# Optimization experiments

Hardware: AMD Instinct MI355X
Metric: run time of the kernel (lower is better)

The kernel has to match this reference:

```python
import jax, jax.numpy as jnp
import numpy as np

B, NPG, D = 512, 200, 256  # graphs, nodes-per-graph, d_model
N = B * NPG
STEP = 4


def setup_inputs() -> dict:
    key = jax.random.key(0)
    ks = jax.random.split(key, 7)
    def xav(k, shape):
        fan_in, fan_out = shape[1], shape[0]
        std = float(np.sqrt(2.0 / (fan_in + fan_out)))
        return jax.random.normal(k, shape, jnp.float32) * std
    return {
        "node": jax.random.normal(ks[0], (N, D), jnp.float32),
        "node_num": jnp.full((B,), NPG, dtype=jnp.int32),
        "W_ih": xav(ks[1], (4 * D, 2 * D)),  # lstm weight_ih_l0
        "W_hh": xav(ks[2], (4 * D, D)),      # lstm weight_hh_l0
        "b_ih": jnp.zeros((4 * D,), jnp.float32),
        "b_hh": jnp.zeros((4 * D,), jnp.float32),
        "Wo": xav(ks[3], (D, 2 * D)),        # W_o.weight
        "bo": jnp.zeros((D,), jnp.float32),  # W_o.bias
    }


def reference(node, node_num, W_ih, W_hh, b_ih, b_hh, Wo, bo):
    n_total, d = node.shape
    bsz = node_num.shape[0]
    batch_idx = jnp.repeat(jnp.arange(bsz), node_num, total_repeat_length=n_total)
    h = jnp.zeros((bsz, d), node.dtype)
    c = jnp.zeros((bsz, d), node.dtype)
    q_star = jnp.zeros((bsz, 2 * d), node.dtype)
    for _ in range(STEP):
        # single-step LSTM (torch gate order: i, f, g, o)
        gates = q_star @ W_ih.T + h @ W_hh.T + b_ih + b_hh
        i, f, g, o = jnp.split(gates, 4, axis=-1)
        c = jax.nn.sigmoid(f) * c + jax.nn.sigmoid(i) * jnp.tanh(g)
        h = jax.nn.sigmoid(o) * jnp.tanh(c)
        q = h  # [B, d]
        # segmented softmax attention over nodes
        e = jnp.sum(node * q[batch_idx], axis=-1)  # [N]
        emax = jax.ops.segment_max(e, batch_idx, num_segments=bsz)
        e = jnp.exp(e - emax[batch_idx])
        denom = jax.ops.segment_sum(e, batch_idx, num_segments=bsz)
        a = e / (denom[batch_idx] + 1e-6)
        r = jax.ops.segment_sum(a[:, None] * node, batch_idx, num_segments=bsz)
        q_star = jnp.concatenate([q, r], axis=-1)
    return q_star @ Wo.T + bo
```

## Files before the change

kernel.cpp:

```cpp
#include <hip/hip_runtime.h>
#include <math.h>

#define DCH 256
#define BSZ 512
#define NPG 200
#define G4  1024
#define K2  512
#define KSD 4

typedef __attribute__((ext_vector_type(8))) short short8v;
typedef __attribute__((ext_vector_type(4))) float f32x4;

__device__ __forceinline__ float sigf(float x) { return 1.0f / (1.0f + __expf(-x)); }

__device__ __forceinline__ unsigned pack2bf(float a, float b) {
    unsigned ua = __float_as_uint(a), ub = __float_as_uint(b);
    ua = (ua + 0x7FFFu + ((ua >> 16) & 1u)) >> 16;
    ub = (ub + 0x7FFFu + ((ub >> 16) & 1u)) & 0xFFFF0000u;
    return ua | ub;
}
__device__ __forceinline__ float lo_bf(unsigned u) { return __uint_as_float(u << 16); }
__device__ __forceinline__ float hi_bf(unsigned u) { return __uint_as_float(u & 0xFFFF0000u); }

__global__ __launch_bounds__(256) void gemm_gates_mfma(
    const unsigned short* __restrict__ hrbf,
    const unsigned short* __restrict__ wcat,
    float* __restrict__ gpart, int Kper)
{
    const int wid  = threadIdx.x >> 6;
    const int lane = threadIdx.x & 63;
    const int gx = blockIdx.x * 128 + wid * 32;
    const int gm = blockIdx.y * 64;
    const int kbase = blockIdx.z * Kper;
    const int rsel = lane & 15, kgrp = lane >> 4;

    f32x4 a0m0 = {}, a0m1 = {}, a0m2 = {}, a0m3 = {},
          a1m0 = {}, a1m1 = {}, a1m2 = {}, a1m3 = {};

    for (int k0 = 0; k0 < Kper; k0 += 32) {
        const int kk = kbase + k0 + kgrp * 8;
        short8v wa0 = *(const short8v*)(wcat + (size_t)(gx +  0 + rsel) * K2 + kk);
        short8v wa1 = *(const short8v*)(wcat + (size_t)(gx + 16 + rsel) * K2 + kk);
        short8v qb0 = *(const short8v*)(hrbf + (size_t)(gm +  0 + rsel) * K2 + kk);
        short8v qb1 = *(const short8v*)(hrbf + (size_t)(gm + 16 + rsel) * K2 + kk);
        short8v qb2 = *(const short8v*)(hrbf + (size_t)(gm + 32 + rsel) * K2 + kk);
        short8v qb3 = *(const short8v*)(hrbf + (size_t)(gm + 48 + rsel) * K2 + kk);
        a0m0 = __builtin_amdgcn_mfma_f32_16x16x32_bf16(wa0, qb0, a0m0, 0, 0, 0);
        a0m1 = __builtin_amdgcn_mfma_f32_16x16x32_bf16(wa0, qb1, a0m1, 0, 0, 0);
        a0m2 = __builtin_amdgcn_mfma_f32_16x16x32_bf16(wa0, qb2, a0m2, 0, 0, 0);
        a0m3 = __builtin_amdgcn_mfma_f32_16x16x32_bf16(wa0, qb3, a0m3, 0, 0, 0);
        a1m0 = __builtin_amdgcn_mfma_f32_16x16x32_bf16(wa1, qb0, a1m0, 0, 0, 0);
        a1m1 = __builtin_amdgcn_mfma_f32_16x16x32_bf16(wa1, qb1, a1m1, 0, 0, 0);
        a1m2 = __builtin_amdgcn_mfma_f32_16x16x32_bf16(wa1, qb2, a1m2, 0, 0, 0);
        a1m3 = __builtin_amdgcn_mfma_f32_16x16x32_bf16(wa1, qb3, a1m3, 0, 0, 0);
    }

    float* Cp = gpart + (size_t)blockIdx.z * BSZ * G4;
    const int gr = kgrp * 4;
    #define STORE_ACC(ni, mi, accv) \
        *(f32x4*)(Cp + (size_t)(gm + (mi)*16 + rsel) * G4 + gx + (ni)*16 + gr) = (accv);
    STORE_ACC(0, 0, a0m0) STORE_ACC(0, 1, a0m1) STORE_ACC(0, 2, a0m2) STORE_ACC(0, 3, a0m3)
    STORE_ACC(1, 0, a1m0) STORE_ACC(1, 1, a1m1) STORE_ACC(1, 2, a1m2) STORE_ACC(1, 3, a1m3)
    #undef STORE_ACC
}

template<int FIRST, int LAST>
__global__ __launch_bounds__(256) void lstm_attn_kernel(
    const float* __restrict__ gpart,
    const float* __restrict__ b_ih, const float* __restrict__ b_hh,
    const float* __restrict__ node, uint4* __restrict__ nbf,
    const int* __restrict__ node_num,
    float* __restrict__ cbuf, unsigned* __restrict__ hrbf,
    const float* __restrict__ W_ih, const float* __restrict__ W_hh,
    const float* __restrict__ Wo,
    uint4* __restrict__ wcat, uint4* __restrict__ wobf,
    const float* __restrict__ bo, float* __restrict__ outp)
{
    __shared__ __align__(16) float smem[4640];
    float* qs = smem;
    float (*red_r)[DCH] = (float (*)[DCH])(smem + 512);
    float* red_m = smem + 4608;
    float* red_s = smem + 4624;

    const int b = blockIdx.x;
    const int t = threadIdx.x;

    if (FIRST) {
        if (t < 160) {
            int idx = blockIdx.x * 160 + t;
            if (idx < 65536) {
                const int n = idx >> 6, k = (idx & 63) * 8;
                float v[8];
                *(float4*)(v)     = *(const float4*)(W_ih + (size_t)n * K2 + k);
                *(float4*)(v + 4) = *(const float4*)(W_ih + (size_t)n * K2 + k + 4);
                if (k < DCH) {
                    float h[8];
                    *(float4*)(h)     = *(const float4*)(W_hh + (size_t)n * DCH + k);
                    *(float4*)(h + 4) = *(const float4*)(W_hh + (size_t)n * DCH + k + 4);
                    #pragma unroll
                    for (int i = 0; i < 8; ++i) v[i] += h[i];
                }
                uint4 u;
                u.x = pack2bf(v[0], v[1]); u.y = pack2bf(v[2], v[3]);
                u.z = pack2bf(v[4], v[5]); u.w = pack2bf(v[6], v[7]);
                wcat[idx] = u;
            } else {
                const int i2 = idx - 65536;
                const int n = i2 >> 6, k = (i2 & 63) * 8;
                float v[8];
                *(float4*)(v)     = *(const float4*)(Wo + (size_t)n * K2 + k);
                *(float4*)(v + 4) = *(const float4*)(Wo + (size_t)n * K2 + k + 4);
                uint4 u;
                u.x = pack2bf(v[0], v[1]); u.y = pack2bf(v[2], v[3]);
                u.z = pack2bf(v[4], v[5]); u.w = pack2bf(v[6], v[7]);
                wobf[i2] = u;
            }
        }
    }

    float gv[4];
    #pragma unroll
    for (int q = 0; q < 4; ++q) {
        const int idx = q * DCH + t;
        float v = b_ih[idx] + b_hh[idx];
        if (!FIRST) {
            #pragma unroll
            for (int z = 0; z < KSD; ++z)
                v += gpart[(size_t)z * BSZ * G4 + (size_t)b * G4 + idx];
        }
        gv[q] = v;
    }
    const float c_old = FIRST ? 0.0f : cbuf[b * DCH + t];
    const float cn = sigf(gv[1]) * c_old + sigf(gv[0]) * tanhf(gv[2]);
    const float hn = sigf(gv[3]) * tanhf(cn);
    if (!LAST) cbuf[b * DCH + t] = cn;
    qs[t] = hn;
    __syncthreads();

    const int w = t >> 6, l = t & 63;
    const int p = l & 15;
    const int g = w * 4 + (l >> 4);
    const int cnt = node_num[b];
    const float* nb = node + (size_t)b * NPG * DCH;
    uint4* nbf_b = nbf + (size_t)b * NPG * 32;

    float4 qv[4];
    #pragma unroll
    for (int j = 0; j < 2; ++j) {
        qv[j*2+0] = *(const float4*)(qs + j * 128 + p * 8);
        qv[j*2+1] = *(const float4*)(qs + j * 128 + p * 8 + 4);
    }

    auto ld = [&](int n, float4* x) {
        if (n < cnt) {
            if (FIRST) {
                #pragma unroll
                for (int j = 0; j < 2; ++j) {
                    x[j*2+0] = *(const float4*)(nb + (size_t)n * DCH + j * 128 + p * 8);
                    x[j*2+1] = *(const float4*)(nb + (size_t)n * DCH + j * 128 + p * 8 + 4);
                }
            } else {
                #pragma unroll
                for (int j = 0; j < 2; ++j) {
                    const uint4 u = nbf_b[(size_t)n * 32 + j * 16 + p];
                    x[j*2+0] = make_float4(lo_bf(u.x), hi_bf(u.x), lo_bf(u.y), hi_bf(u.y));
                    x[j*2+1] = make_float4(lo_bf(u.z), hi_bf(u.z), lo_bf(u.w), hi_bf(u.w));
                }
            }
        } else {
            x[0] = x[1] = x[2] = x[3] = make_float4(0.f, 0.f, 0.f, 0.f);
        }
    };
    auto st_bf = [&](int n, const float4* x) {
        if (n < cnt) {
            #pragma unroll
            for (int j = 0; j < 2; ++j) {
                uint4 u;
                u.x = pack2bf(x[j*2+0].x, x[j*2+0].y);
                u.y = pack2bf(x[j*2+0].z, x[j*2+0].w);
                u.z = pack2bf(x[j*2+1].x, x[j*2+1].y);
                u.w = pack2bf(x[j*2+1].z, x[j*2+1].w);
                nbf_b[(size_t)n * 32 + j * 16 + p] = u;
            }
        }
    };

    float m = -INFINITY, s = 0.0f;
    float4 racc[4] = {};
    const int nit = (cnt + 31) >> 5;

    float4 x0[4], x1[4], u0[4], u1[4];
    ld(2 * g, x0);      ld(2 * g + 1, x1);
    ld(32 + 2 * g, u0); ld(32 + 2 * g + 1, u1);

    for (int it = 0; it < nit; ++it) {
        const int n0 = it * 32 + 2 * g;
        float4 y0[4], y1[4];
        const int np = n0 + 64;
        ld(np, y0); ld(np + 1, y1);
        if (FIRST) { st_bf(n0, x0); st_bf(n0 + 1, x1); }

        float e0 = 0.f, e1 = 0.f;
        #pragma unroll
        for (int j = 0; j < 4; ++j) {
            e0 += x0[j].x * qv[j].x + x0[j].y * qv[j].y + x0[j].z * qv[j].z + x0[j].w * qv[j].w;
            e1 += x1[j].x * qv[j].x + x1[j].y * qv[j].y + x1[j].z * qv[j].z + x1[j].w * qv[j].w;
        }
        #pragma unroll
        for (int off = 1; off < 16; off <<= 1) {
            e0 += __shfl_xor(e0, off);
            e1 += __shfl_xor(e1, off);
        }
        if (n0     >= cnt) e0 = -INFINITY;
        if (n0 + 1 >= cnt) e1 = -INFINITY;
        const float mn = fmaxf(m, fmaxf(e0, e1));
        if (mn > -INFINITY) {
            const float sc = __expf(m - mn);
            const float w0 = __expf(e0 - mn);
            const float w1 = __expf(e1 - mn);
            s = s * sc + w0 + w1;
            #pragma unroll
            for (int j = 0; j < 4; ++j) {
                racc[j].x = racc[j].x * sc + w0 * x0[j].x + w1 * x1[j].x;
                racc[j].y = racc[j].y * sc + w0 * x0[j].y + w1 * x1[j].y;
                racc[j].z = racc[j].z * sc + w0 * x0[j].z + w1 * x1[j].z;
                racc[j].w = racc[j].w * sc + w0 * x0[j].w + w1 * x1[j].w;
            }
            m = mn;
        }
        #pragma unroll
        for (int j = 0; j < 4; ++j) {
            x0[j] = u0[j]; x1[j] = u1[j];
            u0[j] = y0[j]; u1[j] = y1[j];
        }
    }

    #pragma unroll
    for (int j = 0; j < 2; ++j) {
        *(float4*)(&red_r[g][j * 128 + p * 8])     = racc[j*2+0];
        *(float4*)(&red_r[g][j * 128 + p * 8 + 4]) = racc[j*2+1];
    }
    if (p == 0) { red_m[g] = m; red_s[g] = s; }
    __syncthreads();

    float M = -INFINITY;
    #pragma unroll
    for (int g2 = 0; g2 < 16; ++g2) M = fmaxf(M, red_m[g2]);
    float stot = 0.0f, rtot = 0.0f;
    #pragma unroll
    for (int g2 = 0; g2 < 16; ++g2) {
        const float sc = __expf(red_m[g2] - M);
        stot += sc * red_s[g2];
        rtot += sc * red_r[g2][t];
    }
    rtot = rtot / (stot + 1e-6f);

    qs[256 + t] = rtot;
    __syncthreads();

    if (!LAST) {
        hrbf[b * 256 + t] = pack2bf(qs[2 * t], qs[2 * t + 1]);
        return;
    }

    float4 qv2[8];
    #pragma unroll
    for (int j = 0; j < 4; ++j) {
        qv2[j*2+0] = *(const float4*)(qs + j * 128 + p * 8);
        qv2[j*2+1] = *(const float4*)(qs + j * 128 + p * 8 + 4);
    }
    float* out_sm = smem + 512;

    #pragma unroll 2
    for (int v = 0; v < 8; ++v) {
        const int o0 = (2 * v) * 16 + g;
        const int o1 = o0 + 16;
        float e0 = 0.f, e1 = 0.f;
        #pragma unroll
        for (int j = 0; j < 4; ++j) {
            const uint4 ua = wobf[(size_t)o0 * 64 + j * 16 + p];
            const uint4 ub = wobf[(size_t)o1 * 64 + j * 16 + p];
            e0 += lo_bf(ua.x) * qv2[j*2].x + hi_bf(ua.x) * qv2[j*2].y
                + lo_bf(ua.y) * qv2[j*2].z + hi_bf(ua.y) * qv2[j*2].w
                + lo_bf(ua.z) * qv2[j*2+1].x + hi_bf(ua.z) * qv2[j*2+1].y
                + lo_bf(ua.w) * qv2[j*2+1].z + hi_bf(ua.w) * qv2[j*2+1].w;
            e1 += lo_bf(ub.x) * qv2[j*2].x + hi_bf(ub.x) * qv2[j*2].y
                + lo_bf(ub.y) * qv2[j*2].z + hi_bf(ub.y) * qv2[j*2].w
                + lo_bf(ub.z) * qv2[j*2+1].x + hi_bf(ub.z) * qv2[j*2+1].y
                + lo_bf(ub.w) * qv2[j*2+1].z + hi_bf(ub.w) * qv2[j*2+1].w;
        }
        #pragma unroll
        for (int off = 1; off < 16; off <<= 1) {
            e0 += __shfl_xor(e0, off);
            e1 += __shfl_xor(e1, off);
        }
        if (p == 0) {
            out_sm[o0] = e0 + bo[o0];
            out_sm[o1] = e1 + bo[o1];
        }
    }
    __syncthreads();
    outp[(size_t)b * DCH + t] = out_sm[t];
}

extern "C" void kernel_launch(void* const* d_in, const int* in_sizes, int n_in,
                              void* d_out, int out_size, void* d_ws, size_t ws_size,
                              hipStream_t stream)
{
    const float* node     = (const float*)d_in[0];
    const int*   node_num = (const int*)  d_in[1];
    const float* W_ih     = (const float*)d_in[2];
    const float* W_hh     = (const float*)d_in[3];
    const float* b_ih     = (const float*)d_in[4];
    const float* b_hh     = (const float*)d_in[5];
    const float* Wo       = (const float*)d_in[6];
    const float* bo       = (const float*)d_in[7];
    float* out = (float*)d_out;

    float* ws      = (float*)d_ws;
    float* cbuf    = ws;
    unsigned* hrbf = (unsigned*)(cbuf + BSZ * DCH);
    float* gpart   = (float*)(hrbf + BSZ * 256);
    uint4* wcat    = (uint4*)(gpart + (size_t)KSD * BSZ * G4);
    uint4* wobf    = wcat + 1024 * 64;
    uint4* nbf     = wobf + 256 * 64;

    lstm_attn_kernel<1, 0><<<BSZ, 256, 0, stream>>>(
        gpart, b_ih, b_hh, node, nbf, node_num, cbuf, hrbf,
        W_ih, W_hh, Wo, wcat, wobf, bo, out);

    for (int s = 1; s < 4; ++s) {
        gemm_gates_mfma<<<dim3(8, 8, KSD), 256, 0, stream>>>(
            (const unsigned short*)hrbf, (const unsigned short*)wcat, gpart, K2 / KSD);
        if (s < 3) {
            lstm_attn_kernel<0, 0><<<BSZ, 256, 0, stream>>>(
                gpart, b_ih, b_hh, node, nbf, node_num, cbuf, hrbf,
                W_ih, W_hh, Wo, wcat, wobf, bo, out);
        } else {
            lstm_attn_kernel<0, 1><<<BSZ, 256, 0, stream>>>(
                gpart, b_ih, b_hh, node, nbf, node_num, cbuf, hrbf,
                W_ih, W_hh, Wo, wcat, wobf, bo, out);
        }
    }
}
```

Baseline: 100.5 us.

## Fuse all LSTM steps into one persistent kernel with in-block MFMA gate GEMV

Replaces the seven-launch sequence (attention kernels interleaved with split-K gate GEMMs) with a weight-prep kernel plus one kernel in which each 512-thread block handles two graphs across all four steps. Gate pre-activations are computed per block with MFMA against the full bf16 weight matrix, with the two graphs' q_star in the MFMA's B operand. LSTM cell state stays in registers. This removes launch overhead and the global round-trips through gpart, cbuf and hrbf. In exchange, every block re-reads the full 1 MB bf16 weight matrix from cache on each step. Most of each 16-wide MFMA tile is wasted, and only 256 blocks run, each at occupancy 1.

```diff
diff --git a/kernel.cpp b/kernel.cpp
--- a/kernel.cpp
+++ b/kernel.cpp
@@ -6,7 +6,6 @@
 #define NPG 200
 #define G4  1024
 #define K2  512
-#define KSD 4
 
 typedef __attribute__((ext_vector_type(8))) short short8v;
 typedef __attribute__((ext_vector_type(4))) float f32x4;
@@ -22,120 +21,61 @@
 __device__ __forceinline__ float lo_bf(unsigned u) { return __uint_as_float(u << 16); }
 __device__ __forceinline__ float hi_bf(unsigned u) { return __uint_as_float(u & 0xFFFF0000u); }
 
-__global__ __launch_bounds__(256) void gemm_gates_mfma(
-    const unsigned short* __restrict__ hrbf,
-    const unsigned short* __restrict__ wcat,
-    float* __restrict__ gpart, int Kper)
-{
-    const int wid  = threadIdx.x >> 6;
-    const int lane = threadIdx.x & 63;
-    const int gx = blockIdx.x * 128 + wid * 32;
-    const int gm = blockIdx.y * 64;
-    const int kbase = blockIdx.z * Kper;
-    const int rsel = lane & 15, kgrp = lane >> 4;
-
-    f32x4 a0m0 = {}, a0m1 = {}, a0m2 = {}, a0m3 = {},
-          a1m0 = {}, a1m1 = {}, a1m2 = {}, a1m3 = {};
-
-    for (int k0 = 0; k0 < Kper; k0 += 32) {
-        const int kk = kbase + k0 + kgrp * 8;
-        short8v wa0 = *(const short8v*)(wcat + (size_t)(gx +  0 + rsel) * K2 + kk);
-        short8v wa1 = *(const short8v*)(wcat + (size_t)(gx + 16 + rsel) * K2 + kk);
-        short8v qb0 = *(const short8v*)(hrbf + (size_t)(gm +  0 + rsel) * K2 + kk);
-        short8v qb1 = *(const short8v*)(hrbf + (size_t)(gm + 16 + rsel) * K2 + kk);
-        short8v qb2 = *(const short8v*)(hrbf + (size_t)(gm + 32 + rsel) * K2 + kk);
-        short8v qb3 = *(const short8v*)(hrbf + (size_t)(gm + 48 + rsel) * K2 + kk);
-        a0m0 = __builtin_amdgcn_mfma_f32_16x16x32_bf16(wa0, qb0, a0m0, 0, 0, 0);
-        a0m1 = __builtin_amdgcn_mfma_f32_16x16x32_bf16(wa0, qb1, a0m1, 0, 0, 0);
-        a0m2 = __builtin_amdgcn_mfma_f32_16x16x32_bf16(wa0, qb2, a0m2, 0, 0, 0);
-        a0m3 = __builtin_amdgcn_mfma_f32_16x16x32_bf16(wa0, qb3, a0m3, 0, 0, 0);
-        a1m0 = __builtin_amdgcn_mfma_f32_16x16x32_bf16(wa1, qb0, a1m0, 0, 0, 0);
-        a1m1 = __builtin_amdgcn_mfma_f32_16x16x32_bf16(wa1, qb1, a1m1, 0, 0, 0);
-        a1m2 = __builtin_amdgcn_mfma_f32_16x16x32_bf16(wa1, qb2, a1m2, 0, 0, 0);
-        a1m3 = __builtin_amdgcn_mfma_f32_16x16x32_bf16(wa1, qb3, a1m3, 0, 0, 0);
-    }
-
-    float* Cp = gpart + (size_t)blockIdx.z * BSZ * G4;
-    const int gr = kgrp * 4;
-    #define STORE_ACC(ni, mi, accv) \
-        *(f32x4*)(Cp + (size_t)(gm + (mi)*16 + rsel) * G4 + gx + (ni)*16 + gr) = (accv);
-    STORE_ACC(0, 0, a0m0) STORE_ACC(0, 1, a0m1) STORE_ACC(0, 2, a0m2) STORE_ACC(0, 3, a0m3)
-    STORE_ACC(1, 0, a1m0) STORE_ACC(1, 1, a1m1) STORE_ACC(1, 2, a1m2) STORE_ACC(1, 3, a1m3)
-    #undef STORE_ACC
-}
-
-template<int FIRST, int LAST>
-__global__ __launch_bounds__(256) void lstm_attn_kernel(
-    const float* __restrict__ gpart,
-    const float* __restrict__ b_ih, const float* __restrict__ b_hh,
-    const float* __restrict__ node, uint4* __restrict__ nbf,
-    const int* __restrict__ node_num,
-    float* __restrict__ cbuf, unsigned* __restrict__ hrbf,
+__global__ __launch_bounds__(256) void prep_kernel(
     const float* __restrict__ W_ih, const float* __restrict__ W_hh,
     const float* __restrict__ Wo,
-    uint4* __restrict__ wcat, uint4* __restrict__ wobf,
-    const float* __restrict__ bo, float* __restrict__ outp)
+    uint4* __restrict__ wcat, uint4* __restrict__ wobf)
 {
-    __shared__ __align__(16) float smem[4640];
+    int idx = blockIdx.x * 256 + threadIdx.x;
+    if (idx < 65536) {
+        const int n = idx >> 6, k = (idx & 63) * 8;
+        float v[8];
+        *(float4*)(v)     = *(const float4*)(W_ih + (size_t)n * K2 + k);
+        *(float4*)(v + 4) = *(const float4*)(W_ih + (size_t)n * K2 + k + 4);
+        if (k < DCH) {
+            float h[8];
+            *(float4*)(h)     = *(const float4*)(W_hh + (size_t)n * DCH + k);
+            *(float4*)(h + 4) = *(const float4*)(W_hh + (size_t)n * DCH + k + 4);
+            #pragma unroll
+            for (int i = 0; i < 8; ++i) v[i] += h[i];
+        }
+        uint4 u;
+        u.x = pack2bf(v[0], v[1]); u.y = pack2bf(v[2], v[3]);
+        u.z = pack2bf(v[4], v[5]); u.w = pack2bf(v[6], v[7]);
+        wcat[idx] = u;
+    } else {
+        idx -= 65536;
+        const int n = idx >> 6, k = (idx & 63) * 8;
+        float v[8];
+        *(float4*)(v)     = *(const float4*)(Wo + (size_t)n * K2 + k);
+        *(float4*)(v + 4) = *(const float4*)(Wo + (size_t)n * K2 + k + 4);
+        uint4 u;
+        u.x = pack2bf(v[0], v[1]); u.y = pack2bf(v[2], v[3]);
+        u.z = pack2bf(v[4], v[5]); u.w = pack2bf(v[6], v[7]);
+        wobf[idx] = u;
+    }
+}
+
+__global__ void __launch_bounds__(512, 1) mono_kernel(
+    const float* __restrict__ node, const int* __restrict__ node_num,
+    const float* __restrict__ b_ih, const float* __restrict__ b_hh,
+    const unsigned short* __restrict__ wcat, const uint4* __restrict__ wobf,
+    const float* __restrict__ bo,
+    uint4* __restrict__ nbf, float* __restrict__ outp)
+{
+    __shared__ __align__(16) float smem2[2][4640];
+    __shared__ __align__(16) float gatesLDS[2][1024];
+    __shared__ __align__(16) unsigned qsbf[2][256];
+
+    const int tid = threadIdx.x;
+    const int half = tid >> 8, t = tid & 255;
+    const int b = blockIdx.x * 2 + half;
+
+    float* smem = smem2[half];
     float* qs = smem;
     float (*red_r)[DCH] = (float (*)[DCH])(smem + 512);
     float* red_m = smem + 4608;
     float* red_s = smem + 4624;
-
-    const int b = blockIdx.x;
-    const int t = threadIdx.x;
-
-    if (FIRST) {
-        if (t < 160) {
-            int idx = blockIdx.x * 160 + t;
-            if (idx < 65536) {
-                const int n = idx >> 6, k = (idx & 63) * 8;
-                float v[8];
-                *(float4*)(v)     = *(const float4*)(W_ih + (size_t)n * K2 + k);
-                *(float4*)(v + 4) = *(const float4*)(W_ih + (size_t)n * K2 + k + 4);
-                if (k < DCH) {
-                    float h[8];
-                    *(float4*)(h)     = *(const float4*)(W_hh + (size_t)n * DCH + k);
-                    *(float4*)(h + 4) = *(const float4*)(W_hh + (size_t)n * DCH + k + 4);
-                    #pragma unroll
-                    for (int i = 0; i < 8; ++i) v[i] += h[i];
-                }
-                uint4 u;
-                u.x = pack2bf(v[0], v[1]); u.y = pack2bf(v[2], v[3]);
-                u.z = pack2bf(v[4], v[5]); u.w = pack2bf(v[6], v[7]);
-                wcat[idx] = u;
-            } else {
-                const int i2 = idx - 65536;
-                const int n = i2 >> 6, k = (i2 & 63) * 8;
-                float v[8];
-                *(float4*)(v)     = *(const float4*)(Wo + (size_t)n * K2 + k);
-                *(float4*)(v + 4) = *(const float4*)(Wo + (size_t)n * K2 + k + 4);
-                uint4 u;
-                u.x = pack2bf(v[0], v[1]); u.y = pack2bf(v[2], v[3]);
-                u.z = pack2bf(v[4], v[5]); u.w = pack2bf(v[6], v[7]);
-                wobf[i2] = u;
-            }
-        }
-    }
-
-    float gv[4];
-    #pragma unroll
-    for (int q = 0; q < 4; ++q) {
-        const int idx = q * DCH + t;
-        float v = b_ih[idx] + b_hh[idx];
-        if (!FIRST) {
-            #pragma unroll
-            for (int z = 0; z < KSD; ++z)
-                v += gpart[(size_t)z * BSZ * G4 + (size_t)b * G4 + idx];
-        }
-        gv[q] = v;
-    }
-    const float c_old = FIRST ? 0.0f : cbuf[b * DCH + t];
-    const float cn = sigf(gv[1]) * c_old + sigf(gv[0]) * tanhf(gv[2]);
-    const float hn = sigf(gv[3]) * tanhf(cn);
-    if (!LAST) cbuf[b * DCH + t] = cn;
-    qs[t] = hn;
-    __syncthreads();
 
     const int w = t >> 6, l = t & 63;
     const int p = l & 15;
@@ -144,163 +84,209 @@
     const float* nb = node + (size_t)b * NPG * DCH;
     uint4* nbf_b = nbf + (size_t)b * NPG * 32;
 
-    float4 qv[4];
+    const int wv = tid >> 6;
+    const int lane = tid & 63;
+    const int rsel = lane & 15, kgrp = lane >> 4;
+
+    float bsum_r[4];
     #pragma unroll
-    for (int j = 0; j < 2; ++j) {
-        qv[j*2+0] = *(const float4*)(qs + j * 128 + p * 8);
-        qv[j*2+1] = *(const float4*)(qs + j * 128 + p * 8 + 4);
+    for (int q = 0; q < 4; ++q) bsum_r[q] = b_ih[q * DCH + t] + b_hh[q * DCH + t];
+
+    float c_reg = 0.0f;
+
+    for (int s = 0; s < 4; ++s) {
+        if (s > 0) {
+            f32x4 acc[8] = {};
+            const unsigned short* qrow = (const unsigned short*)qsbf[rsel & 1];
+            for (int ks = 0; ks < 16; ++ks) {
+                const int kk = ks * 32 + kgrp * 8;
+                const short8v qb = *(const short8v*)(qrow + kk);
+                #pragma unroll
+                for (int j = 0; j < 8; ++j) {
+                    const int grow = (wv * 8 + j) * 16 + rsel;
+                    const short8v wa = *(const short8v*)(wcat + (size_t)grow * K2 + kk);
+                    acc[j] = __builtin_amdgcn_mfma_f32_16x16x32_bf16(wa, qb, acc[j], 0, 0, 0);
+                }
+            }
+            if (rsel < 2) {
+                #pragma unroll
+                for (int j = 0; j < 8; ++j)
+                    *(f32x4*)(&gatesLDS[rsel][(wv * 8 + j) * 16 + kgrp * 4]) = acc[j];
+            }
+        }
+        __syncthreads();
+
+        float gv[4];
+        #pragma unroll
+        for (int q = 0; q < 4; ++q) {
+            float v = bsum_r[q];
+            if (s > 0) v += gatesLDS[half][q * DCH + t];
+            gv[q] = v;
+        }
+        const float cn = sigf(gv[1]) * c_reg + sigf(gv[0]) * tanhf(gv[2]);
+        const float hn = sigf(gv[3]) * tanhf(cn);
+        c_reg = cn;
+        qs[t] = hn;
+        __syncthreads();
+
+        const bool first = (s == 0);
+        float4 qv[4];
+        #pragma unroll
+        for (int j = 0; j < 2; ++j) {
+            qv[j*2+0] = *(const float4*)(qs + j * 128 + p * 8);
+            qv[j*2+1] = *(const float4*)(qs + j * 128 + p * 8 + 4);
+        }
+
+        auto ld = [&](int n, float4* x) {
+            if (n < cnt) {
+                if (first) {
+                    #pragma unroll
+                    for (int j = 0; j < 2; ++j) {
+                        x[j*2+0] = *(const float4*)(nb + (size_t)n * DCH + j * 128 + p * 8);
+                        x[j*2+1] = *(const float4*)(nb + (size_t)n * DCH + j * 128 + p * 8 + 4);
+                    }
+                } else {
+                    #pragma unroll
+                    for (int j = 0; j < 2; ++j) {
+                        const uint4 u = nbf_b[(size_t)n * 32 + j * 16 + p];
+                        x[j*2+0] = make_float4(lo_bf(u.x), hi_bf(u.x), lo_bf(u.y), hi_bf(u.y));
+                        x[j*2+1] = make_float4(lo_bf(u.z), hi_bf(u.z), lo_bf(u.w), hi_bf(u.w));
+                    }
+                }
+            } else {
+                x[0] = x[1] = x[2] = x[3] = make_float4(0.f, 0.f, 0.f, 0.f);
+            }
+        };
+        auto st_bf = [&](int n, const float4* x) {
+            if (n < cnt) {
+                #pragma unroll
+                for (int j = 0; j < 2; ++j) {
+                    uint4 u;
+                    u.x = pack2bf(x[j*2+0].x, x[j*2+0].y);
+                    u.y = pack2bf(x[j*2+0].z, x[j*2+0].w);
+                    u.z = pack2bf(x[j*2+1].x, x[j*2+1].y);
+                    u.w = pack2bf(x[j*2+1].z, x[j*2+1].w);
+                    nbf_b[(size_t)n * 32 + j * 16 + p] = u;
+                }
+            }
+        };
+
+        float m = -INFINITY, ssum = 0.0f;
+        float4 racc[4] = {};
+        const int nit = (cnt + 31) >> 5;
+
+        float4 x0[4], x1[4], u0[4], u1[4];
+        ld(2 * g, x0);      ld(2 * g + 1, x1);
+        ld(32 + 2 * g, u0); ld(32 + 2 * g + 1, u1);
+
+        for (int it = 0; it < nit; ++it) {
+            const int n0 = it * 32 + 2 * g;
+            float4 y0[4], y1[4];
+            ld(n0 + 64, y0); ld(n0 + 65, y1);
+            if (first) { st_bf(n0, x0); st_bf(n0 + 1, x1); }
+
+            float e0 = 0.f, e1 = 0.f;
+            #pragma unroll
+            for (int j = 0; j < 4; ++j) {
+                e0 += x0[j].x * qv[j].x + x0[j].y * qv[j].y + x0[j].z * qv[j].z + x0[j].w * qv[j].w;
+                e1 += x1[j].x * qv[j].x + x1[j].y * qv[j].y + x1[j].z * qv[j].z + x1[j].w * qv[j].w;
+            }
+            #pragma unroll
+            for (int off = 1; off < 16; off <<= 1) {
+                e0 += __shfl_xor(e0, off);
+                e1 += __shfl_xor(e1, off);
+            }
+            if (n0     >= cnt) e0 = -INFINITY;
+            if (n0 + 1 >= cnt) e1 = -INFINITY;
+            const float mn = fmaxf(m, fmaxf(e0, e1));
+            if (mn > -INFINITY) {
+                const float sc = __expf(m - mn);
+                const float w0 = __expf(e0 - mn);
+                const float w1 = __expf(e1 - mn);
+                ssum = ssum * sc + w0 + w1;
+                #pragma unroll
+                for (int j = 0; j < 4; ++j) {
+                    racc[j].x = racc[j].x * sc + w0 * x0[j].x + w1 * x1[j].x;
+                    racc[j].y = racc[j].y * sc + w0 * x0[j].y + w1 * x1[j].y;
+                    racc[j].z = racc[j].z * sc + w0 * x0[j].z + w1 * x1[j].z;
+                    racc[j].w = racc[j].w * sc + w0 * x0[j].w + w1 * x1[j].w;
+                }
+                m = mn;
+            }
+            #pragma unroll
+            for (int j = 0; j < 4; ++j) {
+                x0[j] = u0[j]; x1[j] = u1[j];
+                u0[j] = y0[j]; u1[j] = y1[j];
+            }
+        }
+
+        #pragma unroll
+        for (int j = 0; j < 2; ++j) {
+            *(float4*)(&red_r[g][j * 128 + p * 8])     = racc[j*2+0];
+            *(float4*)(&red_r[g][j * 128 + p * 8 + 4]) = racc[j*2+1];
+        }
+        if (p == 0) { red_m[g] = m; red_s[g] = ssum; }
+        __syncthreads();
+
+        float M = -INFINITY;
+        #pragma unroll
+        for (int g2 = 0; g2 < 16; ++g2) M = fmaxf(M, red_m[g2]);
+        float stot = 0.0f, rtot = 0.0f;
+        #pragma unroll
+        for (int g2 = 0; g2 < 16; ++g2) {
+            const float sc = __expf(red_m[g2] - M);
+            stot += sc * red_s[g2];
+            rtot += sc * red_r[g2][t];
+        }
+        rtot = rtot / (stot + 1e-6f);
+
+        qs[256 + t] = rtot;
+        __syncthreads();
+
+        if (s < 3) {
+            qsbf[half][t] = pack2bf(qs[2 * t], qs[2 * t + 1]);
+            __syncthreads();
+        } else {
+            float4 qv2[8];
+            #pragma unroll
+            for (int j = 0; j < 4; ++j) {
+                qv2[j*2+0] = *(const float4*)(qs + j * 128 + p * 8);
+                qv2[j*2+1] = *(const float4*)(qs + j * 128 + p * 8 + 4);
+            }
+            float* out_sm = smem + 512;
+
+            #pragma unroll 2
+            for (int v = 0; v < 8; ++v) {
+                const int o0 = (2 * v) * 16 + g;
+                const int o1 = o0 + 16;
+                float e0 = 0.f, e1 = 0.f;
+                #pragma unroll
+                for (int j = 0; j < 4; ++j) {
+                    const uint4 ua = wobf[(size_t)o0 * 64 + j * 16 + p];
+                    const uint4 ub = wobf[(size_t)o1 * 64 + j * 16 + p];
+                    e0 += lo_bf(ua.x) * qv2[j*2].x + hi_bf(ua.x) * qv2[j*2].y
+                        + lo_bf(ua.y) * qv2[j*2].z + hi_bf(ua.y) * qv2[j*2].w
+                        + lo_bf(ua.z) * qv2[j*2+1].x + hi_bf(ua.z) * qv2[j*2+1].y
+                        + lo_bf(ua.w) * qv2[j*2+1].z + hi_bf(ua.w) * qv2[j*2+1].w;
+                    e1 += lo_bf(ub.x) * qv2[j*2].x + hi_bf(ub.x) * qv2[j*2].y
+                        + lo_bf(ub.y) * qv2[j*2].z + hi_bf(ub.y) * qv2[j*2].w
+                        + lo_bf(ub.z) * qv2[j*2+1].x + hi_bf(ub.z) * qv2[j*2+1].y
+                        + lo_bf(ub.w) * qv2[j*2+1].z + hi_bf(ub.w) * qv2[j*2+1].w;
+                }
+                #pragma unroll
+                for (int off = 1; off < 16; off <<= 1) {
+                    e0 += __shfl_xor(e0, off);
+                    e1 += __shfl_xor(e1, off);
+                }
+                if (p == 0) {
+                    out_sm[o0] = e0 + bo[o0];
+                    out_sm[o1] = e1 + bo[o1];
+                }
+            }
+            __syncthreads();
+            outp[(size_t)b * DCH + t] = out_sm[t];
+        }
     }
-
-    auto ld = [&](int n, float4* x) {
-        if (n < cnt) {
-            if (FIRST) {
-                #pragma unroll
-                for (int j = 0; j < 2; ++j) {
-                    x[j*2+0] = *(const float4*)(nb + (size_t)n * DCH + j * 128 + p * 8);
-                    x[j*2+1] = *(const float4*)(nb + (size_t)n * DCH + j * 128 + p * 8 + 4);
-                }
-            } else {
-                #pragma unroll
-                for (int j = 0; j < 2; ++j) {
-                    const uint4 u = nbf_b[(size_t)n * 32 + j * 16 + p];
-                    x[j*2+0] = make_float4(lo_bf(u.x), hi_bf(u.x), lo_bf(u.y), hi_bf(u.y));
-                    x[j*2+1] = make_float4(lo_bf(u.z), hi_bf(u.z), lo_bf(u.w), hi_bf(u.w));
-                }
-            }
-        } else {
-            x[0] = x[1] = x[2] = x[3] = make_float4(0.f, 0.f, 0.f, 0.f);
-        }
-    };
-    auto st_bf = [&](int n, const float4* x) {
-        if (n < cnt) {
-            #pragma unroll
-            for (int j = 0; j < 2; ++j) {
-                uint4 u;
-                u.x = pack2bf(x[j*2+0].x, x[j*2+0].y);
-                u.y = pack2bf(x[j*2+0].z, x[j*2+0].w);
-                u.z = pack2bf(x[j*2+1].x, x[j*2+1].y);
-                u.w = pack2bf(x[j*2+1].z, x[j*2+1].w);
-                nbf_b[(size_t)n * 32 + j * 16 + p] = u;
-            }
-        }
-    };
-
-    float m = -INFINITY, s = 0.0f;
-    float4 racc[4] = {};
-    const int nit = (cnt + 31) >> 5;
-
-    float4 x0[4], x1[4], u0[4], u1[4];
-    ld(2 * g, x0);      ld(2 * g + 1, x1);
-    ld(32 + 2 * g, u0); ld(32 + 2 * g + 1, u1);
-
-    for (int it = 0; it < nit; ++it) {
-        const int n0 = it * 32 + 2 * g;
-        float4 y0[4], y1[4];
-        const int np = n0 + 64;
-        ld(np, y0); ld(np + 1, y1);
-        if (FIRST) { st_bf(n0, x0); st_bf(n0 + 1, x1); }
-
-        float e0 = 0.f, e1 = 0.f;
-        #pragma unroll
-        for (int j = 0; j < 4; ++j) {
-            e0 += x0[j].x * qv[j].x + x0[j].y * qv[j].y + x0[j].z * qv[j].z + x0[j].w * qv[j].w;
-            e1 += x1[j].x * qv[j].x + x1[j].y * qv[j].y + x1[j].z * qv[j].z + x1[j].w * qv[j].w;
-        }
-        #pragma unroll
-        for (int off = 1; off < 16; off <<= 1) {
-            e0 += __shfl_xor(e0, off);
-            e1 += __shfl_xor(e1, off);
-        }
-        if (n0     >= cnt) e0 = -INFINITY;
-        if (n0 + 1 >= cnt) e1 = -INFINITY;
-        const float mn = fmaxf(m, fmaxf(e0, e1));
-        if (mn > -INFINITY) {
-            const float sc = __expf(m - mn);
-            const float w0 = __expf(e0 - mn);
-            const float w1 = __expf(e1 - mn);
-            s = s * sc + w0 + w1;
-            #pragma unroll
-            for (int j = 0; j < 4; ++j) {
-                racc[j].x = racc[j].x * sc + w0 * x0[j].x + w1 * x1[j].x;
-                racc[j].y = racc[j].y * sc + w0 * x0[j].y + w1 * x1[j].y;
-                racc[j].z = racc[j].z * sc + w0 * x0[j].z + w1 * x1[j].z;
-                racc[j].w = racc[j].w * sc + w0 * x0[j].w + w1 * x1[j].w;
-            }
-            m = mn;
-        }
-        #pragma unroll
-        for (int j = 0; j < 4; ++j) {
-            x0[j] = u0[j]; x1[j] = u1[j];
-            u0[j] = y0[j]; u1[j] = y1[j];
-        }
-    }
-
-    #pragma unroll
-    for (int j = 0; j < 2; ++j) {
-        *(float4*)(&red_r[g][j * 128 + p * 8])     = racc[j*2+0];
-        *(float4*)(&red_r[g][j * 128 + p * 8 + 4]) = racc[j*2+1];
-    }
-    if (p == 0) { red_m[g] = m; red_s[g] = s; }
-    __syncthreads();
-
-    float M = -INFINITY;
-    #pragma unroll
-    for (int g2 = 0; g2 < 16; ++g2) M = fmaxf(M, red_m[g2]);
-    float stot = 0.0f, rtot = 0.0f;
-    #pragma unroll
-    for (int g2 = 0; g2 < 16; ++g2) {
-        const float sc = __expf(red_m[g2] - M);
-        stot += sc * red_s[g2];
-        rtot += sc * red_r[g2][t];
-    }
-    rtot = rtot / (stot + 1e-6f);
-
-    qs[256 + t] = rtot;
-    __syncthreads();
-
-    if (!LAST) {
-        hrbf[b * 256 + t] = pack2bf(qs[2 * t], qs[2 * t + 1]);
-        return;
-    }
-
-    float4 qv2[8];
-    #pragma unroll
-    for (int j = 0; j < 4; ++j) {
-        qv2[j*2+0] = *(const float4*)(qs + j * 128 + p * 8);
-        qv2[j*2+1] = *(const float4*)(qs + j * 128 + p * 8 + 4);
-    }
-    float* out_sm = smem + 512;
-
-    #pragma unroll 2
-    for (int v = 0; v < 8; ++v) {
-        const int o0 = (2 * v) * 16 + g;
-        const int o1 = o0 + 16;
-        float e0 = 0.f, e1 = 0.f;
-        #pragma unroll
-        for (int j = 0; j < 4; ++j) {
-            const uint4 ua = wobf[(size_t)o0 * 64 + j * 16 + p];
-            const uint4 ub = wobf[(size_t)o1 * 64 + j * 16 + p];
-            e0 += lo_bf(ua.x) * qv2[j*2].x + hi_bf(ua.x) * qv2[j*2].y
-                + lo_bf(ua.y) * qv2[j*2].z + hi_bf(ua.y) * qv2[j*2].w
-                + lo_bf(ua.z) * qv2[j*2+1].x + hi_bf(ua.z) * qv2[j*2+1].y
-                + lo_bf(ua.w) * qv2[j*2+1].z + hi_bf(ua.w) * qv2[j*2+1].w;
-            e1 += lo_bf(ub.x) * qv2[j*2].x + hi_bf(ub.x) * qv2[j*2].y
-                + lo_bf(ub.y) * qv2[j*2].z + hi_bf(ub.y) * qv2[j*2].w
-                + lo_bf(ub.z) * qv2[j*2+1].x + hi_bf(ub.z) * qv2[j*2+1].y
-                + lo_bf(ub.w) * qv2[j*2+1].z + hi_bf(ub.w) * qv2[j*2+1].w;
-        }
-        #pragma unroll
-        for (int off = 1; off < 16; off <<= 1) {
-            e0 += __shfl_xor(e0, off);
-            e1 += __shfl_xor(e1, off);
-        }
-        if (p == 0) {
-            out_sm[o0] = e0 + bo[o0];
-            out_sm[o1] = e1 + bo[o1];
-        }
-    }
-    __syncthreads();
-    outp[(size_t)b * DCH + t] = out_sm[t];
 }
 
 extern "C" void kernel_launch(void* const* d_in, const int* in_sizes, int n_in,
@@ -317,29 +303,13 @@
     const float* bo       = (const float*)d_in[7];
     float* out = (float*)d_out;
 
-    float* ws      = (float*)d_ws;
-    float* cbuf    = ws;
-    unsigned* hrbf = (unsigned*)(cbuf + BSZ * DCH);
-    float* gpart   = (float*)(hrbf + BSZ * 256);
-    uint4* wcat    = (uint4*)(gpart + (size_t)KSD * BSZ * G4);
-    uint4* wobf    = wcat + 1024 * 64;
-    uint4* nbf     = wobf + 256 * 64;
-
-    lstm_attn_kernel<1, 0><<<BSZ, 256, 0, stream>>>(
-        gpart, b_ih, b_hh, node, nbf, node_num, cbuf, hrbf,
-        W_ih, W_hh, Wo, wcat, wobf, bo, out);
-
-    for (int s = 1; s < 4; ++s) {
-        gemm_gates_mfma<<<dim3(8, 8, KSD), 256, 0, stream>>>(
-            (const unsigned short*)hrbf, (const unsigned short*)wcat, gpart, K2 / KSD);
-        if (s < 3) {
-            lstm_attn_kernel<0, 0><<<BSZ, 256, 0, stream>>>(
-                gpart, b_ih, b_hh, node, nbf, node_num, cbuf, hrbf,
-                W_ih, W_hh, Wo, wcat, wobf, bo, out);
-        } else {
-            lstm_attn_kernel<0, 1><<<BSZ, 256, 0, stream>>>(
-                gpart, b_ih, b_hh, node, nbf, node_num, cbuf, hrbf,
-                W_ih, W_hh, Wo, wcat, wobf, bo, out);
-        }
-    }
+    uint4* wcat = (uint4*)d_ws;
+    uint4* wobf = wcat + 1024 * 64;
+    uint4* nbf  = wobf + 256 * 64;
+
+    prep_kernel<<<320, 256, 0, stream>>>(W_ih, W_hh, Wo, wcat, wobf);
+
+    mono_kernel<<<BSZ / 2, 512, 0, stream>>>(
+        node, node_num, b_ih, b_hh,
+        (const unsigned short*)wcat, wobf, bo, nbf, out);
 }
```

Result: slower. 254.6 us (+153.3%).

## Split first attention step across four node slices with separate merge kernel

Applied to the files above, without the earlier changes.

The first LSTM+attention step, which reads the fp32 node tensor and writes its bf16 copy, now runs over 2048 blocks, each handling 50 nodes of one graph. Each block writes partial softmax max, sum and weighted sums, and a new merge kernel combines them, computes the step-1 LSTM state and packs the bf16 q_star. This targets the bandwidth-bound first pass, which had only 512 blocks and long serial loops per graph. It costs an extra kernel launch and a small round trip of partial results through global memory.

```diff
diff --git a/kernel.cpp b/kernel.cpp
--- a/kernel.cpp
+++ b/kernel.cpp
@@ -7,6 +7,8 @@
 #define G4  1024
 #define K2  512
 #define KSD 4
+#define NSL 4
+#define SLN 50
 
 typedef __attribute__((ext_vector_type(8))) short short8v;
 typedef __attribute__((ext_vector_type(4))) float f32x4;
@@ -64,17 +66,15 @@
     #undef STORE_ACC
 }
 
-template<int FIRST, int LAST>
-__global__ __launch_bounds__(256) void lstm_attn_kernel(
-    const float* __restrict__ gpart,
+__global__ __launch_bounds__(256) void attn1_part_kernel(
+    const float* __restrict__ node, const int* __restrict__ node_num,
     const float* __restrict__ b_ih, const float* __restrict__ b_hh,
-    const float* __restrict__ node, uint4* __restrict__ nbf,
-    const int* __restrict__ node_num,
-    float* __restrict__ cbuf, unsigned* __restrict__ hrbf,
     const float* __restrict__ W_ih, const float* __restrict__ W_hh,
     const float* __restrict__ Wo,
     uint4* __restrict__ wcat, uint4* __restrict__ wobf,
-    const float* __restrict__ bo, float* __restrict__ outp)
+    uint4* __restrict__ nbf,
+    float* __restrict__ r_part, float* __restrict__ m_part,
+    float* __restrict__ s_part)
 {
     __shared__ __align__(16) float smem[4640];
     float* qs = smem;
@@ -82,65 +82,57 @@
     float* red_m = smem + 4608;
     float* red_s = smem + 4624;
 
-    const int b = blockIdx.x;
+    const int bid = blockIdx.x;
+    const int b = bid >> 2, sl = bid & 3;
     const int t = threadIdx.x;
 
-    if (FIRST) {
-        if (t < 160) {
-            int idx = blockIdx.x * 160 + t;
-            if (idx < 65536) {
-                const int n = idx >> 6, k = (idx & 63) * 8;
-                float v[8];
-                *(float4*)(v)     = *(const float4*)(W_ih + (size_t)n * K2 + k);
-                *(float4*)(v + 4) = *(const float4*)(W_ih + (size_t)n * K2 + k + 4);
-                if (k < DCH) {
-                    float h[8];
-                    *(float4*)(h)     = *(const float4*)(W_hh + (size_t)n * DCH + k);
-                    *(float4*)(h + 4) = *(const float4*)(W_hh + (size_t)n * DCH + k + 4);
-                    #pragma unroll
-                    for (int i = 0; i < 8; ++i) v[i] += h[i];
-                }
-                uint4 u;
-                u.x = pack2bf(v[0], v[1]); u.y = pack2bf(v[2], v[3]);
-                u.z = pack2bf(v[4], v[5]); u.w = pack2bf(v[6], v[7]);
-                wcat[idx] = u;
-            } else {
-                const int i2 = idx - 65536;
-                const int n = i2 >> 6, k = (i2 & 63) * 8;
-                float v[8];
-                *(float4*)(v)     = *(const float4*)(Wo + (size_t)n * K2 + k);
-                *(float4*)(v + 4) = *(const float4*)(Wo + (size_t)n * K2 + k + 4);
-                uint4 u;
-                u.x = pack2bf(v[0], v[1]); u.y = pack2bf(v[2], v[3]);
-                u.z = pack2bf(v[4], v[5]); u.w = pack2bf(v[6], v[7]);
-                wobf[i2] = u;
-            }
-        }
-    }
-
-    float gv[4];
-    #pragma unroll
-    for (int q = 0; q < 4; ++q) {
-        const int idx = q * DCH + t;
-        float v = b_ih[idx] + b_hh[idx];
-        if (!FIRST) {
-            #pragma unroll
-            for (int z = 0; z < KSD; ++z)
-                v += gpart[(size_t)z * BSZ * G4 + (size_t)b * G4 + idx];
-        }
-        gv[q] = v;
-    }
-    const float c_old = FIRST ? 0.0f : cbuf[b * DCH + t];
-    const float cn = sigf(gv[1]) * c_old + sigf(gv[0]) * tanhf(gv[2]);
-    const float hn = sigf(gv[3]) * tanhf(cn);
-    if (!LAST) cbuf[b * DCH + t] = cn;
-    qs[t] = hn;
+    if (t < 40) {
+        int idx = bid * 40 + t;
+        if (idx < 65536) {
+            const int n = idx >> 6, k = (idx & 63) * 8;
+            float v[8];
+            *(float4*)(v)     = *(const float4*)(W_ih + (size_t)n * K2 + k);
+            *(float4*)(v + 4) = *(const float4*)(W_ih + (size_t)n * K2 + k + 4);
+            if (k < DCH) {
+                float h[8];
+                *(float4*)(h)     = *(const float4*)(W_hh + (size_t)n * DCH + k);
+                *(float4*)(h + 4) = *(const float4*)(W_hh + (size_t)n * DCH + k + 4);
+                #pragma unroll
+                for (int i = 0; i < 8; ++i) v[i] += h[i];
+            }
+            uint4 u;
+            u.x = pack2bf(v[0], v[1]); u.y = pack2bf(v[2], v[3]);
+            u.z = pack2bf(v[4], v[5]); u.w = pack2bf(v[6], v[7]);
+            wcat[idx] = u;
+        } else {
+            const int i2 = idx - 65536;
+            const int n = i2 >> 6, k = (i2 & 63) * 8;
+            float v[8];
+            *(float4*)(v)     = *(const float4*)(Wo + (size_t)n * K2 + k);
+            *(float4*)(v + 4) = *(const float4*)(Wo + (size_t)n * K2 + k + 4);
+            uint4 u;
+            u.x = pack2bf(v[0], v[1]); u.y = pack2bf(v[2], v[3]);
+            u.z = pack2bf(v[4], v[5]); u.w = pack2bf(v[6], v[7]);
+            wobf[i2] = u;
+        }
+    }
+
+    {
+        float gv[4];
+        #pragma unroll
+        for (int q = 0; q < 4; ++q) gv[q] = b_ih[q * DCH + t] + b_hh[q * DCH + t];
+        const float cn = sigf(gv[0]) * tanhf(gv[2]);
+        const float hn = sigf(gv[3]) * tanhf(cn);
+        qs[t] = hn;
+    }
     __syncthreads();
 
     const int w = t >> 6, l = t & 63;
     const int p = l & 15;
     const int g = w * 4 + (l >> 4);
     const int cnt = node_num[b];
+    const int lo = sl * SLN;
+    const int hi = min(lo + SLN, cnt);
     const float* nb = node + (size_t)b * NPG * DCH;
     uint4* nbf_b = nbf + (size_t)b * NPG * 32;
 
@@ -152,27 +144,18 @@
     }
 
     auto ld = [&](int n, float4* x) {
-        if (n < cnt) {
-            if (FIRST) {
-                #pragma unroll
-                for (int j = 0; j < 2; ++j) {
-                    x[j*2+0] = *(const float4*)(nb + (size_t)n * DCH + j * 128 + p * 8);
-                    x[j*2+1] = *(const float4*)(nb + (size_t)n * DCH + j * 128 + p * 8 + 4);
-                }
-            } else {
-                #pragma unroll
-                for (int j = 0; j < 2; ++j) {
-                    const uint4 u = nbf_b[(size_t)n * 32 + j * 16 + p];
-                    x[j*2+0] = make_float4(lo_bf(u.x), hi_bf(u.x), lo_bf(u.y), hi_bf(u.y));
-                    x[j*2+1] = make_float4(lo_bf(u.z), hi_bf(u.z), lo_bf(u.w), hi_bf(u.w));
-                }
+        if (n < hi) {
+            #pragma unroll
+            for (int j = 0; j < 2; ++j) {
+                x[j*2+0] = *(const float4*)(nb + (size_t)n * DCH + j * 128 + p * 8);
+                x[j*2+1] = *(const float4*)(nb + (size_t)n * DCH + j * 128 + p * 8 + 4);
             }
         } else {
             x[0] = x[1] = x[2] = x[3] = make_float4(0.f, 0.f, 0.f, 0.f);
         }
     };
     auto st_bf = [&](int n, const float4* x) {
-        if (n < cnt) {
+        if (n < hi) {
             #pragma unroll
             for (int j = 0; j < 2; ++j) {
                 uint4 u;
@@ -185,7 +168,175 @@
         }
     };
 
-    float m = -INFINITY, s = 0.0f;
+    float m = -INFINITY, ssum = 0.0f;
+    float4 racc[4] = {};
+    const int span = hi - lo;
+    const int nit = (span > 0) ? ((span + 31) >> 5) : 0;
+
+    float4 x0[4], x1[4], u0[4], u1[4];
+    ld(lo + 2 * g, x0);      ld(lo + 2 * g + 1, x1);
+    ld(lo + 32 + 2 * g, u0); ld(lo + 32 + 2 * g + 1, u1);
+
+    for (int it = 0; it < nit; ++it) {
+        const int n0 = lo + it * 32 + 2 * g;
+        float4 y0[4], y1[4];
+        ld(n0 + 64, y0); ld(n0 + 65, y1);
+        st_bf(n0, x0); st_bf(n0 + 1, x1);
+
+        float e0 = 0.f, e1 = 0.f;
+        #pragma unroll
+        for (int j = 0; j < 4; ++j) {
+            e0 += x0[j].x * qv[j].x + x0[j].y * qv[j].y + x0[j].z * qv[j].z + x0[j].w * qv[j].w;
+            e1 += x1[j].x * qv[j].x + x1[j].y * qv[j].y + x1[j].z * qv[j].z + x1[j].w * qv[j].w;
+        }
+        #pragma unroll
+        for (int off = 1; off < 16; off <<= 1) {
+            e0 += __shfl_xor(e0, off);
+            e1 += __shfl_xor(e1, off);
+        }
+        if (n0     >= hi) e0 = -INFINITY;
+        if (n0 + 1 >= hi) e1 = -INFINITY;
+        const float mn = fmaxf(m, fmaxf(e0, e1));
+        if (mn > -INFINITY) {
+            const float sc = __expf(m - mn);
+            const float w0 = __expf(e0 - mn);
+            const float w1 = __expf(e1 - mn);
+            ssum = ssum * sc + w0 + w1;
+            #pragma unroll
+            for (int j = 0; j < 4; ++j) {
+                racc[j].x = racc[j].x * sc + w0 * x0[j].x + w1 * x1[j].x;
+                racc[j].y = racc[j].y * sc + w0 * x0[j].y + w1 * x1[j].y;
+                racc[j].z = racc[j].z * sc + w0 * x0[j].z + w1 * x1[j].z;
+                racc[j].w = racc[j].w * sc + w0 * x0[j].w + w1 * x1[j].w;
+            }
+            m = mn;
+        }
+        #pragma unroll
+        for (int j = 0; j < 4; ++j) {
+            x0[j] = u0[j]; x1[j] = u1[j];
+            u0[j] = y0[j]; u1[j] = y1[j];
+        }
+    }
+
+    #pragma unroll
+    for (int j = 0; j < 2; ++j) {
+        *(float4*)(&red_r[g][j * 128 + p * 8])     = racc[j*2+0];
+        *(float4*)(&red_r[g][j * 128 + p * 8 + 4]) = racc[j*2+1];
+    }
+    if (p == 0) { red_m[g] = m; red_s[g] = ssum; }
+    __syncthreads();
+
+    float M = -INFINITY;
+    #pragma unroll
+    for (int g2 = 0; g2 < 16; ++g2) M = fmaxf(M, red_m[g2]);
+    float stot = 0.0f, rtot = 0.0f;
+    if (M > -INFINITY) {
+        #pragma unroll
+        for (int g2 = 0; g2 < 16; ++g2) {
+            const float sc = __expf(red_m[g2] - M);
+            stot += sc * red_s[g2];
+            rtot += sc * red_r[g2][t];
+        }
+    }
+    if (t == 0) { m_part[bid] = M; s_part[bid] = stot; }
+    else if (t == 1) s_part[bid] = stot;
+    r_part[(size_t)bid * DCH + t] = rtot;
+}
+
+__global__ __launch_bounds__(256) void attn1_merge_kernel(
+    const float* __restrict__ r_part, const float* __restrict__ m_part,
+    const float* __restrict__ s_part,
+    const float* __restrict__ b_ih, const float* __restrict__ b_hh,
+    float* __restrict__ cbuf, unsigned* __restrict__ hrbf)
+{
+    __shared__ __align__(16) float qsm[512];
+    const int b = blockIdx.x, t = threadIdx.x;
+
+    float gv[4];
+    #pragma unroll
+    for (int q = 0; q < 4; ++q) gv[q] = b_ih[q * DCH + t] + b_hh[q * DCH + t];
+    const float cn = sigf(gv[0]) * tanhf(gv[2]);
+    const float hn = sigf(gv[3]) * tanhf(cn);
+    cbuf[b * DCH + t] = cn;
+    qsm[t] = hn;
+
+    float M = -INFINITY;
+    #pragma unroll
+    for (int ps = 0; ps < NSL; ++ps) M = fmaxf(M, m_part[b * NSL + ps]);
+    float stot = 0.0f, rtot = 0.0f;
+    #pragma unroll
+    for (int ps = 0; ps < NSL; ++ps) {
+        const float sc = __expf(m_part[b * NSL + ps] - M);
+        stot += sc * s_part[b * NSL + ps];
+        rtot += sc * r_part[(size_t)(b * NSL + ps) * DCH + t];
+    }
+    qsm[256 + t] = rtot / (stot + 1e-6f);
+    __syncthreads();
+    hrbf[b * 256 + t] = pack2bf(qsm[2 * t], qsm[2 * t + 1]);
+}
+
+template<int LAST>
+__global__ __launch_bounds__(256) void lstm_attn_kernel(
+    const float* __restrict__ gpart,
+    const float* __restrict__ b_ih, const float* __restrict__ b_hh,
+    const uint4* __restrict__ nbf, const int* __restrict__ node_num,
+    float* __restrict__ cbuf, unsigned* __restrict__ hrbf,
+    const uint4* __restrict__ wobf, const float* __restrict__ bo,
+    float* __restrict__ outp)
+{
+    __shared__ __align__(16) float smem[4640];
+    float* qs = smem;
+    float (*red_r)[DCH] = (float (*)[DCH])(smem + 512);
+    float* red_m = smem + 4608;
+    float* red_s = smem + 4624;
+
+    const int b = blockIdx.x;
+    const int t = threadIdx.x;
+
+    float gv[4];
+    #pragma unroll
+    for (int q = 0; q < 4; ++q) {
+        const int idx = q * DCH + t;
+        float v = b_ih[idx] + b_hh[idx];
+        #pragma unroll
+        for (int z = 0; z < KSD; ++z)
+            v += gpart[(size_t)z * BSZ * G4 + (size_t)b * G4 + idx];
+        gv[q] = v;
+    }
+    const float c_old = cbuf[b * DCH + t];
+    const float cn = sigf(gv[1]) * c_old + sigf(gv[0]) * tanhf(gv[2]);
+    const float hn = sigf(gv[3]) * tanhf(cn);
+    if (!LAST) cbuf[b * DCH + t] = cn;
+    qs[t] = hn;
+    __syncthreads();
+
+    const int w = t >> 6, l = t & 63;
+    const int p = l & 15;
+    const int g = w * 4 + (l >> 4);
+    const int cnt = node_num[b];
+    const uint4* nbf_b = nbf + (size_t)b * NPG * 32;
+
+    float4 qv[4];
+    #pragma unroll
+    for (int j = 0; j < 2; ++j) {
+        qv[j*2+0] = *(const float4*)(qs + j * 128 + p * 8);
+        qv[j*2+1] = *(const float4*)(qs + j * 128 + p * 8 + 4);
+    }
+
+    auto ld = [&](int n, float4* x) {
+        if (n < cnt) {
+            #pragma unroll
+            for (int j = 0; j < 2; ++j) {
+                const uint4 u = nbf_b[(size_t)n * 32 + j * 16 + p];
+                x[j*2+0] = make_float4(lo_bf(u.x), hi_bf(u.x), lo_bf(u.y), hi_bf(u.y));
+                x[j*2+1] = make_float4(lo_bf(u.z), hi_bf(u.z), lo_bf(u.w), hi_bf(u.w));
+            }
+        } else {
+            x[0] = x[1] = x[2] = x[3] = make_float4(0.f, 0.f, 0.f, 0.f);
+        }
+    };
+
+    float m = -INFINITY, ssum = 0.0f;
     float4 racc[4] = {};
     const int nit = (cnt + 31) >> 5;
 
@@ -196,9 +347,7 @@
     for (int it = 0; it < nit; ++it) {
         const int n0 = it * 32 + 2 * g;
         float4 y0[4], y1[4];
-        const int np = n0 + 64;
-        ld(np, y0); ld(np + 1, y1);
-        if (FIRST) { st_bf(n0, x0); st_bf(n0 + 1, x1); }
+        ld(n0 + 64, y0); ld(n0 + 65, y1);
 
         float e0 = 0.f, e1 = 0.f;
         #pragma unroll
@@ -218,7 +367,7 @@
             const float sc = __expf(m - mn);
             const float w0 = __expf(e0 - mn);
             const float w1 = __expf(e1 - mn);
-            s = s * sc + w0 + w1;
+            ssum = ssum * sc + w0 + w1;
             #pragma unroll
             for (int j = 0; j < 4; ++j) {
                 racc[j].x = racc[j].x * sc + w0 * x0[j].x + w1 * x1[j].x;
@@ -240,7 +389,7 @@
         *(float4*)(&red_r[g][j * 128 + p * 8])     = racc[j*2+0];
         *(float4*)(&red_r[g][j * 128 + p * 8 + 4]) = racc[j*2+1];
     }
-    if (p == 0) { red_m[g] = m; red_s[g] = s; }
+    if (p == 0) { red_m[g] = m; red_s[g] = ssum; }
     __syncthreads();
 
     float M = -INFINITY;
@@ -323,23 +472,26 @@
     float* gpart   = (float*)(hrbf + BSZ * 256);
     uint4* wcat    = (uint4*)(gpart + (size_t)KSD * BSZ * G4);
     uint4* wobf    = wcat + 1024 * 64;
-    uint4* nbf     = wobf + 256 * 64;
-
-    lstm_attn_kernel<1, 0><<<BSZ, 256, 0, stream>>>(
-        gpart, b_ih, b_hh, node, nbf, node_num, cbuf, hrbf,
-        W_ih, W_hh, Wo, wcat, wobf, bo, out);
+    float* m_part  = (float*)(wobf + 256 * 64);
+    float* s_part  = m_part + BSZ * NSL;
+    float* r_part  = s_part + BSZ * NSL;
+    uint4* nbf     = (uint4*)(r_part + (size_t)BSZ * NSL * DCH);
+
+    attn1_part_kernel<<<BSZ * NSL, 256, 0, stream>>>(
+        node, node_num, b_ih, b_hh, W_ih, W_hh, Wo,
+        wcat, wobf, nbf, r_part, m_part, s_part);
+    attn1_merge_kernel<<<BSZ, 256, 0, stream>>>(
+        r_part, m_part, s_part, b_ih, b_hh, cbuf, hrbf);
 
     for (int s = 1; s < 4; ++s) {
         gemm_gates_mfma<<<dim3(8, 8, KSD), 256, 0, stream>>>(
             (const unsigned short*)hrbf, (const unsigned short*)wcat, gpart, K2 / KSD);
         if (s < 3) {
-            lstm_attn_kernel<0, 0><<<BSZ, 256, 0, stream>>>(
-                gpart, b_ih, b_hh, node, nbf, node_num, cbuf, hrbf,
-                W_ih, W_hh, Wo, wcat, wobf, bo, out);
+            lstm_attn_kernel<0><<<BSZ, 256, 0, stream>>>(
+                gpart, b_ih, b_hh, nbf, node_num, cbuf, hrbf, wobf, bo, out);
         } else {
-            lstm_attn_kernel<0, 1><<<BSZ, 256, 0, stream>>>(
-                gpart, b_ih, b_hh, node, nbf, node_num, cbuf, hrbf,
-                W_ih, W_hh, Wo, wcat, wobf, bo, out);
-        }
-    }
-}
+            lstm_attn_kernel<1><<<BSZ, 256, 0, stream>>>(
+                gpart, b_ih, b_hh, nbf, node_num, cbuf, hrbf, wobf, bo, out);
+        }
+    }
+}
```

Result: slower. 105.4 us (+4.9%).
